# Kernel tuning notes

Hardware: AMD Instinct MI355X
Metric: run time of the kernel (lower is better)

Reference implementation:

```python
import jax, jax.numpy as jnp
import numpy as np

DIM = 512
HEADS = 8
HEAD_DIM = DIM // HEADS
SCALE = HEAD_DIM ** -0.5
CPB_HIDDEN = 512
N_CLASSES = 2
LN_EPS = 1e-5


def _layernorm(x, g, b):
    m = jnp.mean(x, axis=-1, keepdims=True)
    v = jnp.var(x, axis=-1, keepdims=True)
    return (x - m) / jnp.sqrt(v + LN_EPS) * g + b


def _coord_attention(x, coords, cpb_w1, cpb_b1, cpb_w2, cpb_b2, qkv_w, qkv_b, proj_w, proj_b):
    B, N, C = x.shape
    qkv = (x @ qkv_w + qkv_b).reshape(B, N, 3, HEADS, HEAD_DIM)
    q, k, v = jnp.moveaxis(qkv, 2, 0)  # each (B, N, H, hd)
    attn = jnp.einsum('bnhd,bmhd->bhnm', q * SCALE, k)  # (B, H, N, N)
    rel = coords[:, :, None, :] - coords[:, None, :, :]  # (B, N, N, 2)
    rel = rel / (jnp.linalg.norm(rel, axis=-1, keepdims=True) + 1e-6)
    bias = jax.nn.relu(rel @ cpb_w1 + cpb_b1) @ cpb_w2 + cpb_b2  # (B, N, N, H)
    attn = jax.nn.softmax(attn + jnp.transpose(bias, (0, 3, 1, 2)), axis=-1)
    out = jnp.einsum('bhnm,bmhd->bnhd', attn, v).reshape(B, N, C)
    return out @ proj_w + proj_b


def setup_inputs() -> dict:
    key = jax.random.key(0)
    ks = iter(jax.random.split(key, 32))
    d = {}
    d['h'] = jax.random.normal(next(ks), (1, 400, 1024), dtype=jnp.float32)
    d['coords'] = jax.random.uniform(next(ks), (1, 400, 2), dtype=jnp.float32) * 1000.0
    def lin(kw, kb, fan_in, fan_out):
        w = jax.random.normal(kw, (fan_in, fan_out), dtype=jnp.float32) / np.sqrt(fan_in)
        b = jax.random.normal(kb, (fan_out,), dtype=jnp.float32) * 0.01
        return w, b
    d['fc1_w'], d['fc1_b'] = lin(next(ks), next(ks), 1024, DIM)
    d['cls_token'] = jax.random.normal(next(ks), (1, 1, DIM), dtype=jnp.float32)
    for p in ('l1', 'l2'):
        d[p + '_norm_g'] = jnp.ones((DIM,), jnp.float32)
        d[p + '_norm_b'] = jnp.zeros((DIM,), jnp.float32)
        d[p + '_cpb_w1'], d[p + '_cpb_b1'] = lin(next(ks), next(ks), 2, CPB_HIDDEN)
        d[p + '_cpb_w2'], d[p + '_cpb_b2'] = lin(next(ks), next(ks), CPB_HIDDEN, HEADS)
        d[p + '_qkv_w'], d[p + '_qkv_b'] = lin(next(ks), next(ks), DIM, 3 * DIM)
        d[p + '_proj_w'], d[p + '_proj_b'] = lin(next(ks), next(ks), DIM, DIM)
    d['norm_g'] = jnp.ones((DIM,), jnp.float32)
    d['norm_b'] = jnp.zeros((DIM,), jnp.float32)
    d['fc2_w'], d['fc2_b'] = lin(next(ks), next(ks), DIM, N_CLASSES)
    return d


def reference(h, coords, fc1_w, fc1_b, cls_token,
              l1_norm_g, l1_norm_b, l1_cpb_w1, l1_cpb_b1, l1_cpb_w2, l1_cpb_b2,
              l1_qkv_w, l1_qkv_b, l1_proj_w, l1_proj_b,
              l2_norm_g, l2_norm_b, l2_cpb_w1, l2_cpb_b1, l2_cpb_w2, l2_cpb_b2,
              l2_qkv_w, l2_qkv_b, l2_proj_w, l2_proj_b,
              norm_g, norm_b, fc2_w, fc2_b):
    B, Np, _ = h.shape
    h = jax.nn.relu(h @ fc1_w + fc1_b)  # (B, N, 512)
    side = int(np.ceil(np.sqrt(Np)))
    add = side * side - Np  # pad bag to a perfect square (wrap-around copy)
    h = jnp.concatenate([h, h[:, :add, :]], axis=1)
    coords = jnp.concatenate([coords, coords[:, :add, :]], axis=1)
    cls = jnp.broadcast_to(cls_token, (B, 1, DIM))
    h = jnp.concatenate([cls, h], axis=1)
    coords = jnp.concatenate([jnp.zeros((B, 1, 2), h.dtype), coords], axis=1)
    h = h + _coord_attention(_layernorm(h, l1_norm_g, l1_norm_b), coords,
                             l1_cpb_w1, l1_cpb_b1, l1_cpb_w2, l1_cpb_b2,
                             l1_qkv_w, l1_qkv_b, l1_proj_w, l1_proj_b)
    h = h + _coord_attention(_layernorm(h, l2_norm_g, l2_norm_b), coords,
                             l2_cpb_w1, l2_cpb_b1, l2_cpb_w2, l2_cpb_b2,
                             l2_qkv_w, l2_qkv_b, l2_proj_w, l2_proj_b)
    h = _layernorm(h, norm_g, norm_b)[:, 0]  # CLS token
    return h @ fc2_w + fc2_b  # (B, n_classes)
```

## Files before the change

kernel.cpp:

```cpp
#include <hip/hip_runtime.h>
#include <math.h>

#define NP 401
#define DIM 512
#define LN_EPS 1e-5f
#define ATT_SCALE 0.125f
#define SP 448
#define PLANE (NP * SP)
#define CPB_M 16384
#define TSTRIDE (CPB_M + 64)
#define PQS (401L * 1536)
#define PVS (401L * 512)

template<bool TB, typename LA, typename LB>
__device__ __forceinline__ void gemm64(
    int kBeg, int kEnd, int tid,
    float (*as)[68], float (*bs)[68], float (&acc)[4][4],
    LA&& loadA, LB&& loadB)
{
    float aR[4], bR[4];
    loadA(kBeg, aR);
    loadB(kBeg, bR);
    for (int k0 = kBeg; k0 < kEnd; k0 += 16) {
        const int arow = tid >> 2, aq = tid & 3;
        as[aq * 4 + 0][arow] = aR[0];
        as[aq * 4 + 1][arow] = aR[1];
        as[aq * 4 + 2][arow] = aR[2];
        as[aq * 4 + 3][arow] = aR[3];
        if (!TB) {
            *(float4*)&bs[tid >> 4][(tid & 15) * 4] =
                make_float4(bR[0], bR[1], bR[2], bR[3]);
        } else {
            bs[aq * 4 + 0][arow] = bR[0];
            bs[aq * 4 + 1][arow] = bR[1];
            bs[aq * 4 + 2][arow] = bR[2];
            bs[aq * 4 + 3][arow] = bR[3];
        }
        __syncthreads();
        float nA[4] = {0.f,0.f,0.f,0.f}, nB[4] = {0.f,0.f,0.f,0.f};
        if (k0 + 16 < kEnd) { loadA(k0 + 16, nA); loadB(k0 + 16, nB); }
        const int tx = tid & 15, ty = tid >> 4;
        #pragma unroll
        for (int kk = 0; kk < 16; ++kk) {
            float4 a4 = *(const float4*)&as[kk][ty * 4];
            float4 b4 = *(const float4*)&bs[kk][tx * 4];
            float av[4] = {a4.x, a4.y, a4.z, a4.w};
            float bv[4] = {b4.x, b4.y, b4.z, b4.w};
            #pragma unroll
            for (int r = 0; r < 4; ++r)
                #pragma unroll
                for (int c = 0; c < 4; ++c)
                    acc[r][c] = fmaf(av[r], bv[c], acc[r][c]);
        }
        __syncthreads();
        #pragma unroll
        for (int j = 0; j < 4; ++j) { aR[j] = nA[j]; bR[j] = nB[j]; }
    }
}

__global__ __launch_bounds__(256) void gemm_split_kernel(
    const float* __restrict__ A, int lda,
    const float* __restrict__ B, int ldb,
    float* __restrict__ P, int ldc, long slice,
    int M, int N, int K, int skN)
{
    __shared__ float as[16][68], bs[16][68];
    const int tid = threadIdx.x;
    const int m0 = blockIdx.x * 64, n0 = blockIdx.y * 64;
    const int sk = blockIdx.z;
    const int KS = ((K + skN * 16 - 1) / (skN * 16)) * 16;
    const int kBeg = sk * KS;
    const int kEnd = (kBeg + KS < K) ? kBeg + KS : K;
    float acc[4][4] = {};

    auto loadA = [&](int k0, float r[4]) {
        r[0] = r[1] = r[2] = r[3] = 0.f;
        int gm = m0 + (tid >> 2);
        if (gm >= M) return;
        int gk = k0 + (tid & 3) * 4;
        const float* p = A + (long)gm * lda + gk;
        if (gk + 3 < kEnd) {
            float4 v = *(const float4*)p;
            r[0] = v.x; r[1] = v.y; r[2] = v.z; r[3] = v.w;
        } else {
            #pragma unroll
            for (int j = 0; j < 4; ++j) if (gk + j < kEnd) r[j] = p[j];
        }
    };
    auto loadB = [&](int k0, float r[4]) {
        r[0] = r[1] = r[2] = r[3] = 0.f;
        int gk = k0 + (tid >> 4);
        if (gk >= kEnd) return;
        int gn = n0 + (tid & 15) * 4;
        const float* p = B + (long)gk * ldb + gn;
        float4 v = *(const float4*)p;
        r[0] = v.x; r[1] = v.y; r[2] = v.z; r[3] = v.w;
    };
    if (kBeg < kEnd)
        gemm64<false>(kBeg, kEnd, tid, as, bs, acc, loadA, loadB);

    float* C = P + (long)sk * slice;
    const int tx = tid & 15, ty = tid >> 4;
    #pragma unroll
    for (int r = 0; r < 4; ++r) {
        int m = m0 + ty * 4 + r;
        if (m >= M) continue;
        *(float4*)&C[(long)m * ldc + n0 + tx * 4] =
            make_float4(acc[r][0], acc[r][1], acc[r][2], acc[r][3]);
    }
}

__global__ __launch_bounds__(256) void qk_kernel(
    const float* __restrict__ Pq, const float* __restrict__ qkvb,
    const int* __restrict__ pm, const float* __restrict__ pf,
    const float* __restrict__ T, float* __restrict__ S)
{
    __shared__ float as[16][68], bs[16][68];
    const int tid = threadIdx.x;
    const int m0 = blockIdx.x * 64, n0 = blockIdx.y * 64, h = blockIdx.z;
    float acc[4][4] = {};

    auto loadQ = [&](int k0, float r[4]) {
        int gm = m0 + (tid >> 2);
        if (gm > 400) { r[0]=r[1]=r[2]=r[3]=0.f; return; }
        int gk = k0 + (tid & 3) * 4;
        long off = (long)gm * 1536 + h * 64 + gk;
        float4 x0 = *(const float4*)(Pq + off);
        float4 x1 = *(const float4*)(Pq + PQS + off);
        float4 x2 = *(const float4*)(Pq + 2 * PQS + off);
        float4 x3 = *(const float4*)(Pq + 3 * PQS + off);
        float4 b  = *(const float4*)(qkvb + h * 64 + gk);
        r[0] = x0.x + x1.x + x2.x + x3.x + b.x;
        r[1] = x0.y + x1.y + x2.y + x3.y + b.y;
        r[2] = x0.z + x1.z + x2.z + x3.z + b.z;
        r[3] = x0.w + x1.w + x2.w + x3.w + b.w;
    };
    auto loadK = [&](int k0, float r[4]) {
        int gn = n0 + (tid >> 2);
        if (gn > 400) { r[0]=r[1]=r[2]=r[3]=0.f; return; }
        int gk = k0 + (tid & 3) * 4;
        long off = (long)gn * 1536 + 512 + h * 64 + gk;
        float4 x0 = *(const float4*)(Pq + off);
        float4 x1 = *(const float4*)(Pq + PQS + off);
        float4 x2 = *(const float4*)(Pq + 2 * PQS + off);
        float4 x3 = *(const float4*)(Pq + 3 * PQS + off);
        float4 b  = *(const float4*)(qkvb + 512 + h * 64 + gk);
        r[0] = x0.x + x1.x + x2.x + x3.x + b.x;
        r[1] = x0.y + x1.y + x2.y + x3.y + b.y;
        r[2] = x0.z + x1.z + x2.z + x3.z + b.z;
        r[3] = x0.w + x1.w + x2.w + x3.w + b.w;
    };
    gemm64<true>(0, 64, tid, as, bs, acc, loadQ, loadK);

    const int tx = tid & 15, ty = tid >> 4;
    const float* Tt = T + (long)h * TSTRIDE;
    float* Sp = S + (long)h * PLANE;
    #pragma unroll
    for (int r = 0; r < 4; ++r) {
        int i = m0 + ty * 4 + r;
        if (i > 400) continue;
        #pragma unroll
        for (int c = 0; c < 4; ++c) {
            int j = n0 + tx * 4 + c;
            if (j > 400) continue;
            int id = i * 416 + j;
            int mm = pm[id];
            float fr = pf[id];
            float t0 = Tt[mm], t1 = Tt[mm + 1];
            Sp[(long)i * SP + j] =
                fmaf(acc[r][c], ATT_SCALE, fmaf(fr, t1 - t0, t0));
        }
    }
}

__global__ __launch_bounds__(256) void softmax_kernel(float* __restrict__ S)
{
    int r = blockIdx.x * 4 + (threadIdx.x >> 6);
    if (r >= 3208) return;
    int hh = r / 401, i = r - hh * 401;
    float* row = S + (long)hh * PLANE + (long)i * SP;
    int lane = threadIdx.x & 63;
    float v[7], mx = -INFINITY;
    #pragma unroll
    for (int j = 0; j < 7; ++j) {
        int c = lane + j * 64;
        v[j] = (c < NP) ? row[c] : -INFINITY;
        mx = fmaxf(mx, v[j]);
    }
    #pragma unroll
    for (int off = 32; off > 0; off >>= 1)
        mx = fmaxf(mx, __shfl_xor(mx, off));
    float s = 0.f;
    #pragma unroll
    for (int j = 0; j < 7; ++j) {
        v[j] = (lane + j * 64 < NP) ? __expf(v[j] - mx) : 0.f;
        s += v[j];
    }
    #pragma unroll
    for (int off = 32; off > 0; off >>= 1)
        s += __shfl_xor(s, off);
    float inv = 1.f / s;
    #pragma unroll
    for (int j = 0; j < 7; ++j) {
        int c = lane + j * 64;
        if (c < NP) row[c] = v[j] * inv;
    }
}

__global__ __launch_bounds__(256) void pv_kernel(
    const float* __restrict__ S, const float* __restrict__ Pq,
    const float* __restrict__ qkvb, float* __restrict__ Pv)
{
    __shared__ float as[16][68], bs[16][68];
    const int tid = threadIdx.x;
    const int m0 = blockIdx.x * 64;
    const int h = blockIdx.z >> 2, sk = blockIdx.z & 3;
    const int kBeg = sk * 112;
    const int kEnd = (kBeg + 112 < NP) ? kBeg + 112 : NP;
    float acc[4][4] = {};

    auto loadA = [&](int k0, float r[4]) {
        r[0] = r[1] = r[2] = r[3] = 0.f;
        int gm = m0 + (tid >> 2);
        if (gm > 400) return;
        int gk = k0 + (tid & 3) * 4;
        const float* p = S + (long)h * PLANE + (long)gm * SP + gk;
        if (gk + 3 < kEnd) {
            float4 v = *(const float4*)p;
            r[0]=v.x; r[1]=v.y; r[2]=v.z; r[3]=v.w;
        } else {
            #pragma unroll
            for (int j = 0; j < 4; ++j) if (gk + j < kEnd) r[j] = p[j];
        }
    };
    auto loadB = [&](int k0, float r[4]) {
        r[0] = r[1] = r[2] = r[3] = 0.f;
        int key = k0 + (tid >> 4);
        if (key >= kEnd) return;
        int d = (tid & 15) * 4;
        long off = (long)key * 1536 + 1024 + h * 64 + d;
        float4 x0 = *(const float4*)(Pq + off);
        float4 x1 = *(const float4*)(Pq + PQS + off);
        float4 x2 = *(const float4*)(Pq + 2 * PQS + off);
        float4 x3 = *(const float4*)(Pq + 3 * PQS + off);
        float4 b  = *(const float4*)(qkvb + 1024 + h * 64 + d);
        r[0] = x0.x + x1.x + x2.x + x3.x + b.x;
        r[1] = x0.y + x1.y + x2.y + x3.y + b.y;
        r[2] = x0.z + x1.z + x2.z + x3.z + b.z;
        r[3] = x0.w + x1.w + x2.w + x3.w + b.w;
    };
    gemm64<false>(kBeg, kEnd, tid, as, bs, acc, loadA, loadB);

    float* C = Pv + (long)sk * PVS;
    const int tx = tid & 15, ty = tid >> 4;
    #pragma unroll
    for (int r = 0; r < 4; ++r) {
        int m = m0 + ty * 4 + r;
        if (m > 400) continue;
        *(float4*)&C[(long)m * 512 + h * 64 + tx * 4] =
            make_float4(acc[r][0], acc[r][1], acc[r][2], acc[r][3]);
    }
}

__global__ __launch_bounds__(256) void proj_kernel(
    const float* __restrict__ Pv, const float* __restrict__ projw,
    float* __restrict__ Pp)
{
    __shared__ float as[16][68], bs[16][68];
    const int tid = threadIdx.x;
    const int m0 = blockIdx.x * 64, n0 = blockIdx.y * 64, sk = blockIdx.z;
    const int kBeg = sk * 64, kEnd = kBeg + 64;
    float acc[4][4] = {};

    auto loadA = [&](int k0, float r[4]) {
        r[0] = r[1] = r[2] = r[3] = 0.f;
        int gm = m0 + (tid >> 2);
        if (gm > 400) return;
        int gk = k0 + (tid & 3) * 4;
        long off = (long)gm * 512 + gk;
        float4 x0 = *(const float4*)(Pv + off);
        float4 x1 = *(const float4*)(Pv + PVS + off);
        float4 x2 = *(const float4*)(Pv + 2 * PVS + off);
        float4 x3 = *(const float4*)(Pv + 3 * PVS + off);
        r[0] = x0.x + x1.x + x2.x + x3.x;
        r[1] = x0.y + x1.y + x2.y + x3.y;
        r[2] = x0.z + x1.z + x2.z + x3.z;
        r[3] = x0.w + x1.w + x2.w + x3.w;
    };
    auto loadB = [&](int k0, float r[4]) {
        int gk = k0 + (tid >> 4);
        int gn = n0 + (tid & 15) * 4;
        float4 v = *(const float4*)(projw + (long)gk * 512 + gn);
        r[0]=v.x; r[1]=v.y; r[2]=v.z; r[3]=v.w;
    };
    gemm64<false>(kBeg, kEnd, tid, as, bs, acc, loadA, loadB);

    float* C = Pp + (long)sk * PVS;
    const int tx = tid & 15, ty = tid >> 4;
    #pragma unroll
    for (int r = 0; r < 4; ++r) {
        int m = m0 + ty * 4 + r;
        if (m > 400) continue;
        *(float4*)&C[(long)m * 512 + n0 + tx * 4] =
            make_float4(acc[r][0], acc[r][1], acc[r][2], acc[r][3]);
    }
}

__global__ __launch_bounds__(256) void rowfuse_kernel(
    const float* __restrict__ P, long slice, int skN, int rowOff,
    const float* __restrict__ bias, int doRelu,
    const float* __restrict__ resid, const float* __restrict__ cls,
    float* __restrict__ h0,
    const float* __restrict__ g, const float* __restrict__ b,
    float* __restrict__ xln)
{
    const int r = blockIdx.x, t = threadIdx.x;
    float v0, v1;
    if (cls && r == 0) {
        v0 = cls[t]; v1 = cls[t + 256];
    } else {
        const float* p = P + (long)(r - rowOff) * DIM;
        v0 = bias[t]; v1 = bias[t + 256];
        for (int k = 0; k < skN; ++k) {
            v0 += p[(long)k * slice + t];
            v1 += p[(long)k * slice + t + 256];
        }
        if (resid) {
            v0 += resid[(long)r * DIM + t];
            v1 += resid[(long)r * DIM + t + 256];
        }
        if (doRelu) { v0 = fmaxf(v0, 0.f); v1 = fmaxf(v1, 0.f); }
    }
    h0[(long)r * DIM + t] = v0;
    h0[(long)r * DIM + t + 256] = v1;

    float s = v0 + v1, sq = v0 * v0 + v1 * v1;
    #pragma unroll
    for (int off = 32; off > 0; off >>= 1) {
        s += __shfl_down(s, off);
        sq += __shfl_down(sq, off);
    }
    __shared__ float ps[4], pq[4];
    int w = t >> 6, lane = t & 63;
    if (lane == 0) { ps[w] = s; pq[w] = sq; }
    __syncthreads();
    float Sm = ps[0] + ps[1] + ps[2] + ps[3];
    float Q = pq[0] + pq[1] + pq[2] + pq[3];
    float mean = Sm * (1.f / DIM);
    float var = Q * (1.f / DIM) - mean * mean;
    float inv = rsqrtf(var + LN_EPS);
    xln[(long)r * DIM + t]       = (v0 - mean) * inv * g[t] + b[t];
    xln[(long)r * DIM + t + 256] = (v1 - mean) * inv * g[t + 256] + b[t + 256];
}

__global__ __launch_bounds__(256) void cls_decode_kernel(
    const float* __restrict__ Pq, const float* __restrict__ qkvb,
    const int* __restrict__ pm, const float* __restrict__ pf,
    const float* __restrict__ T,
    float* __restrict__ cms, float* __restrict__ cpv)
{
    const int h = blockIdx.x, c = blockIdx.y, tid = threadIdx.x;
    const int kBeg = c * 64;
    __shared__ float q0[64], scraw[64], p[64], red[4][64], rr[2];

    if (tid < 64) {
        long o = h * 64 + tid;
        q0[tid] = Pq[o] + Pq[PQS + o] + Pq[2 * PQS + o] + Pq[3 * PQS + o]
                  + qkvb[o];
    }
    __syncthreads();

    {
        int k = tid >> 2, q = tid & 3;
        int j = kBeg + k;
        float dot = 0.f;
        if (j < NP) {
            long base = (long)j * 1536 + 512 + h * 64 + q * 16;
            #pragma unroll
            for (int d = 0; d < 16; d += 4) {
                float4 x0 = *(const float4*)(Pq + base + d);
                float4 x1 = *(const float4*)(Pq + PQS + base + d);
                float4 x2 = *(const float4*)(Pq + 2 * PQS + base + d);
                float4 x3 = *(const float4*)(Pq + 3 * PQS + base + d);
                float4 bb = *(const float4*)(qkvb + 512 + h * 64 + q * 16 + d);
                float4 qq = *(const float4*)(q0 + q * 16 + d);
                dot = fmaf(qq.x, x0.x + x1.x + x2.x + x3.x + bb.x, dot);
                dot = fmaf(qq.y, x0.y + x1.y + x2.y + x3.y + bb.y, dot);
                dot = fmaf(qq.z, x0.z + x1.z + x2.z + x3.z + bb.z, dot);
                dot = fmaf(qq.w, x0.w + x1.w + x2.w + x3.w + bb.w, dot);
            }
        }
        dot += __shfl_down(dot, 2);
        dot += __shfl_down(dot, 1);
        if (q == 0) scraw[k] = dot;
    }
    __syncthreads();

    if (tid < 64) {
        int j = kBeg + tid;
        float s;
        if (j < NP) {
            int mm = pm[j];
            float fr = pf[j];
            const float* Tt = T + (long)h * TSTRIDE;
            float t0 = Tt[mm], t1 = Tt[mm + 1];
            s = fmaf(scraw[tid], ATT_SCALE, fmaf(fr, t1 - t0, t0));
        } else {
            s = -INFINITY;
        }
        float m = s;
        #pragma unroll
        for (int off = 32; off > 0; off >>= 1)
            m = fmaxf(m, __shfl_xor(m, off));
        float e = (j < NP) ? __expf(s - m) : 0.f;
        float sum = e;
        #pragma unroll
        for (int off = 32; off > 0; off >>= 1)
            sum += __shfl_xor(sum, off);
        p[tid] = e;
        if (tid == 0) { rr[0] = m; rr[1] = sum; }
    }
    __syncthreads();

    {
        int w = tid >> 6, d = tid & 63;
        float vb = qkvb[1024 + h * 64 + d];
        float acc = 0.f;
        for (int k = w; k < 64; k += 4) {
            int j = kBeg + k;
            if (j >= NP) break;
            long o = (long)j * 1536 + 1024 + h * 64 + d;
            float v = Pq[o] + Pq[PQS + o] + Pq[2 * PQS + o] + Pq[3 * PQS + o]
                      + vb;
            acc = fmaf(p[k], v, acc);
        }
        red[w][d] = acc;
    }
    __syncthreads();
    if (tid < 64) {
        cpv[((long)h * 7 + c) * 64 + tid] =
            red[0][tid] + red[1][tid] + red[2][tid] + red[3][tid];
        if (tid == 0) {
            cms[(h * 7 + c) * 2 + 0] = rr[0];
            cms[(h * 7 + c) * 2 + 1] = rr[1];
        }
    }
}

__global__ __launch_bounds__(64) void cls_combine_kernel(
    const float* __restrict__ cms, const float* __restrict__ cpv,
    float* __restrict__ att0)
{
    int h = blockIdx.x, d = threadIdx.x;
    float M = -INFINITY;
    #pragma unroll
    for (int c = 0; c < 7; ++c)
        M = fmaxf(M, cms[(h * 7 + c) * 2]);
    float S = 0.f, acc = 0.f;
    #pragma unroll
    for (int c = 0; c < 7; ++c) {
        float e = __expf(cms[(h * 7 + c) * 2] - M);
        S += cms[(h * 7 + c) * 2 + 1] * e;
        acc += cpv[((long)h * 7 + c) * 64 + d] * e;
    }
    att0[h * 64 + d] = acc / S;
}

__global__ __launch_bounds__(256) void cls_proj_kernel(
    const float* __restrict__ att0, const float* __restrict__ projw,
    const float* __restrict__ projb, float* __restrict__ proj0)
{
    __shared__ float av[512], red[4][64];
    const int b = blockIdx.x, tid = threadIdx.x;
    av[tid] = att0[tid];
    av[tid + 256] = att0[tid + 256];
    __syncthreads();
    int g = tid >> 6, n = b * 64 + (tid & 63);
    float acc = 0.f;
    for (int k = g * 128; k < g * 128 + 128; ++k)
        acc = fmaf(av[k], projw[(long)k * 512 + n], acc);
    red[g][tid & 63] = acc;
    __syncthreads();
    if (tid < 64)
        proj0[b * 64 + tid] = red[0][tid] + red[1][tid] + red[2][tid]
                              + red[3][tid] + projb[b * 64 + tid];
}

__global__ __launch_bounds__(256) void cls_out_kernel(
    const float* __restrict__ h0, const float* __restrict__ proj0,
    const float* __restrict__ g, const float* __restrict__ b,
    const float* __restrict__ fc2w, const float* __restrict__ fc2b,
    float* __restrict__ out)
{
    const int t = threadIdx.x;
    float v0 = h0[t] + proj0[t];
    float v1 = h0[t + 256] + proj0[t + 256];
    float s = v0 + v1, sq = v0 * v0 + v1 * v1;
    #pragma unroll
    for (int off = 32; off > 0; off >>= 1) {
        s += __shfl_down(s, off);
        sq += __shfl_down(sq, off);
    }
    __shared__ float ps[4], pq[4], pc0[4], pc1[4];
    int w = t >> 6, lane = t & 63;
    if (lane == 0) { ps[w] = s; pq[w] = sq; }
    __syncthreads();
    float Sm = ps[0] + ps[1] + ps[2] + ps[3];
    float Q = pq[0] + pq[1] + pq[2] + pq[3];
    float mean = Sm * (1.f / DIM);
    float var = Q * (1.f / DIM) - mean * mean;
    float inv = rsqrtf(var + LN_EPS);
    float n0 = (v0 - mean) * inv * g[t] + b[t];
    float n1 = (v1 - mean) * inv * g[t + 256] + b[t + 256];
    float c0 = n0 * fc2w[t * 2]     + n1 * fc2w[(t + 256) * 2];
    float c1 = n0 * fc2w[t * 2 + 1] + n1 * fc2w[(t + 256) * 2 + 1];
    #pragma unroll
    for (int off = 32; off > 0; off >>= 1) {
        c0 += __shfl_down(c0, off);
        c1 += __shfl_down(c1, off);
    }
    if (lane == 0) { pc0[w] = c0; pc1[w] = c1; }
    __syncthreads();
    if (t == 0) {
        out[0] = pc0[0] + pc0[1] + pc0[2] + pc0[3] + fc2b[0];
        out[1] = pc1[0] + pc1[1] + pc1[2] + pc1[3] + fc2b[1];
    }
}

__global__ __launch_bounds__(256) void mega_kernel(
    const float* __restrict__ hin, const float* __restrict__ fc1_w,
    const float* __restrict__ w1_0, const float* __restrict__ b1_0,
    const float* __restrict__ w2_0, const float* __restrict__ b2_0,
    const float* __restrict__ w1_1, const float* __restrict__ b1_1,
    const float* __restrict__ w2_1, const float* __restrict__ b2_1,
    const float* __restrict__ coords,
    float* __restrict__ Pp, float* __restrict__ T,
    int* __restrict__ pm, float* __restrict__ pf)
{
    __shared__ float smem[2176];
    float (*as)[68] = (float(*)[68])smem;
    float (*bs)[68] = (float(*)[68])(smem + 1088);
    float (*red)[64][8] = (float(*)[64][8])smem;
    const int bid = blockIdx.x, tid = threadIdx.x;

    if (bid < 896) {
        int sk = bid / 56, rem = bid % 56;
        int m0 = (rem % 7) * 64, n0 = (rem / 7) * 64;
        int kBeg = sk * 64, kEnd = kBeg + 64;
        float acc[4][4] = {};
        auto loadA = [&](int k0, float r[4]) {
            r[0]=r[1]=r[2]=r[3]=0.f;
            int gm = m0 + (tid >> 2);
            if (gm >= 400) return;
            int gk = k0 + (tid & 3) * 4;
            float4 v = *(const float4*)(hin + (long)gm * 1024 + gk);
            r[0]=v.x; r[1]=v.y; r[2]=v.z; r[3]=v.w;
        };
        auto loadB = [&](int k0, float r[4]) {
            int gk = k0 + (tid >> 4);
            int gn = n0 + (tid & 15) * 4;
            float4 v = *(const float4*)(fc1_w + (long)gk * 512 + gn);
            r[0]=v.x; r[1]=v.y; r[2]=v.z; r[3]=v.w;
        };
        gemm64<false>(kBeg, kEnd, tid, as, bs, acc, loadA, loadB);
        float* C = Pp + (long)sk * PVS;
        const int tx = tid & 15, ty = tid >> 4;
        #pragma unroll
        for (int r = 0; r < 4; ++r) {
            int m = m0 + ty * 4 + r;
            if (m >= 400) continue;
            *(float4*)&C[(long)m * 512 + n0 + tx * 4] =
                make_float4(acc[r][0], acc[r][1], acc[r][2], acc[r][3]);
        }
    } else if (bid < 1410) {
        int tb = bid - 896;
        int z = tb / 257, ab = tb % 257;
        const float* w1 = z ? w1_1 : w1_0;
        const float* b1 = z ? b1_1 : b1_0;
        const float* w2 = z ? w2_1 : w2_0;
        const float* b2 = z ? b2_1 : b2_0;
        const int lane = tid & 63, wv = tid >> 6;
        float ca = 0.f, sa = 0.f;
        if (ab != 256) {
            float th = fmaf((float)(ab * 64 + lane),
                            (float)(2.0 * M_PI / CPB_M), -(float)M_PI);
            sincosf(th, &sa, &ca);
        } else if (lane == 0) {
            sincosf((float)M_PI, &sa, &ca);
        }
        float a8[8] = {};
        const int kbeg = wv * 128;
        #pragma unroll 4
        for (int k = kbeg; k < kbeg + 128; ++k) {
            float hk = fmaxf(fmaf(ca, w1[k],
                                  fmaf(sa, w1[512 + k], b1[k])), 0.f);
            #pragma unroll
            for (int h2 = 0; h2 < 8; ++h2)
                a8[h2] = fmaf(hk, w2[k * 8 + h2], a8[h2]);
        }
        #pragma unroll
        for (int h2 = 0; h2 < 8; ++h2) red[wv][lane][h2] = a8[h2];
        __syncthreads();
        if (tid < 64) {
            int aidx = ab * 64 + tid;
            #pragma unroll
            for (int h2 = 0; h2 < 8; ++h2)
                T[(long)(z * 8 + h2) * TSTRIDE + aidx] =
                    red[0][tid][h2] + red[1][tid][h2] +
                    red[2][tid][h2] + red[3][tid][h2] + b2[h2];
        }
    } else {
        int p = (bid - 1410) * 256 + tid;
        if (p < NP * NP) {
            int i = p / NP, j = p - i * NP;
            float xi = (i == 0) ? 0.f : coords[(i - 1) * 2];
            float yi = (i == 0) ? 0.f : coords[(i - 1) * 2 + 1];
            float xj = (j == 0) ? 0.f : coords[(j - 1) * 2];
            float yj = (j == 0) ? 0.f : coords[(j - 1) * 2 + 1];
            float rx = xi - xj, ry = yi - yj;
            int mm; float fr;
            if (rx == 0.f && ry == 0.f) {
                mm = CPB_M + 1; fr = 0.f;
            } else {
                float x = (atan2f(ry, rx) + 3.14159265358979f)
                          * (float)(CPB_M / (2.0 * M_PI));
                int mi = (int)x;
                fr = x - (float)mi;
                mm = (mi >= CPB_M) ? mi - CPB_M : mi;
            }
            pm[i * 416 + j] = mm;
            pf[i * 416 + j] = fr;
        }
    }
}

extern "C" void kernel_launch(void* const* d_in, const int* in_sizes, int n_in,
                              void* d_out, int out_size, void* d_ws, size_t ws_size,
                              hipStream_t stream)
{
    const float* coords = (const float*)d_in[1];
    float* ws = (float*)d_ws;
    float* h0   = ws;                    ws += 401L * 512;
    float* xln  = ws;                    ws += 401L * 512;
    float* S    = ws;                    ws += 8L * PLANE;
    float* T    = ws;                    ws += 16L * TSTRIDE;
    int*   pm   = (int*)ws;              ws += 401L * 416;
    float* pf   = ws;                    ws += 401L * 416;
    float* Pq   = ws;                    ws += 4L * PQS;
    float* Pv   = ws;                    ws += 4L * PVS;
    float* Pp   = ws;                    ws += 16L * PVS;
    float* att0 = ws;                    ws += 512;
    float* proj0 = ws;                   ws += 512;
    float* cms  = ws;                    ws += 8L * 7 * 2;
    float* cpv  = ws;                    ws += 8L * 7 * 64;

    mega_kernel<<<2039, 256, 0, stream>>>(
        (const float*)d_in[0], (const float*)d_in[2],
        (const float*)d_in[7],  (const float*)d_in[8],
        (const float*)d_in[9],  (const float*)d_in[10],
        (const float*)d_in[17], (const float*)d_in[18],
        (const float*)d_in[19], (const float*)d_in[20],
        coords, Pp, T, pm, pf);

    rowfuse_kernel<<<401, 256, 0, stream>>>(
        Pp, PVS, 16, 1, (const float*)d_in[3], 1, nullptr,
        (const float*)d_in[4], h0,
        (const float*)d_in[5], (const float*)d_in[6], xln);

    gemm_split_kernel<<<dim3(7, 24, 4), 256, 0, stream>>>(
        xln, 512, (const float*)d_in[11], 1536, Pq, 1536, PQS,
        401, 1536, 512, 4);
    qk_kernel<<<dim3(7, 7, 8), 256, 0, stream>>>(
        Pq, (const float*)d_in[12], pm, pf, T, S);
    softmax_kernel<<<802, 256, 0, stream>>>(S);
    pv_kernel<<<dim3(7, 1, 32), 256, 0, stream>>>(
        S, Pq, (const float*)d_in[12], Pv);
    proj_kernel<<<dim3(7, 8, 8), 256, 0, stream>>>(
        Pv, (const float*)d_in[13], Pp);
    rowfuse_kernel<<<401, 256, 0, stream>>>(
        Pp, PVS, 8, 0, (const float*)d_in[14], 0, h0, nullptr, h0,
        (const float*)d_in[15], (const float*)d_in[16], xln);

    gemm_split_kernel<<<dim3(7, 24, 4), 256, 0, stream>>>(
        xln, 512, (const float*)d_in[21], 1536, Pq, 1536, PQS,
        401, 1536, 512, 4);
    cls_decode_kernel<<<dim3(8, 7), 256, 0, stream>>>(
        Pq, (const float*)d_in[22], pm, pf, T + 8L * TSTRIDE, cms, cpv);
    cls_combine_kernel<<<8, 64, 0, stream>>>(cms, cpv, att0);
    cls_proj_kernel<<<8, 256, 0, stream>>>(
        att0, (const float*)d_in[23], (const float*)d_in[24], proj0);
    cls_out_kernel<<<1, 256, 0, stream>>>(
        h0, proj0, (const float*)d_in[25], (const float*)d_in[26],
        (const float*)d_in[27], (const float*)d_in[28], (float*)d_out);
}
```

Baseline: 263.9 us.

## Reduce split-K partials once in a dedicated kernel; fold cls combine into proj

```diff
diff --git a/kernel.cpp b/kernel.cpp
--- a/kernel.cpp
+++ b/kernel.cpp
@@ -110,8 +110,27 @@
     }
 }
 
+__global__ __launch_bounds__(256) void reduce_kernel(
+    const float* __restrict__ P, long slice, int skN,
+    const float* __restrict__ bias, float* __restrict__ out,
+    int total, int N)
+{
+    int idx = (blockIdx.x * 256 + threadIdx.x) * 4;
+    if (idx >= total) return;
+    float4 s = *(const float4*)(P + idx);
+    for (int k = 1; k < skN; ++k) {
+        float4 p = *(const float4*)(P + (long)k * slice + idx);
+        s.x += p.x; s.y += p.y; s.z += p.z; s.w += p.w;
+    }
+    if (bias) {
+        const float4 b = *(const float4*)(bias + (idx % N));
+        s.x += b.x; s.y += b.y; s.z += b.z; s.w += b.w;
+    }
+    *(float4*)(out + idx) = s;
+}
+
 __global__ __launch_bounds__(256) void qk_kernel(
-    const float* __restrict__ Pq, const float* __restrict__ qkvb,
+    const float* __restrict__ qkv,
     const int* __restrict__ pm, const float* __restrict__ pf,
     const float* __restrict__ T, float* __restrict__ S)
 {
@@ -124,31 +143,15 @@
         int gm = m0 + (tid >> 2);
         if (gm > 400) { r[0]=r[1]=r[2]=r[3]=0.f; return; }
         int gk = k0 + (tid & 3) * 4;
-        long off = (long)gm * 1536 + h * 64 + gk;
-        float4 x0 = *(const float4*)(Pq + off);
-        float4 x1 = *(const float4*)(Pq + PQS + off);
-        float4 x2 = *(const float4*)(Pq + 2 * PQS + off);
-        float4 x3 = *(const float4*)(Pq + 3 * PQS + off);
-        float4 b  = *(const float4*)(qkvb + h * 64 + gk);
-        r[0] = x0.x + x1.x + x2.x + x3.x + b.x;
-        r[1] = x0.y + x1.y + x2.y + x3.y + b.y;
-        r[2] = x0.z + x1.z + x2.z + x3.z + b.z;
-        r[3] = x0.w + x1.w + x2.w + x3.w + b.w;
+        float4 v = *(const float4*)(qkv + (long)gm * 1536 + h * 64 + gk);
+        r[0]=v.x; r[1]=v.y; r[2]=v.z; r[3]=v.w;
     };
     auto loadK = [&](int k0, float r[4]) {
         int gn = n0 + (tid >> 2);
         if (gn > 400) { r[0]=r[1]=r[2]=r[3]=0.f; return; }
         int gk = k0 + (tid & 3) * 4;
-        long off = (long)gn * 1536 + 512 + h * 64 + gk;
-        float4 x0 = *(const float4*)(Pq + off);
-        float4 x1 = *(const float4*)(Pq + PQS + off);
-        float4 x2 = *(const float4*)(Pq + 2 * PQS + off);
-        float4 x3 = *(const float4*)(Pq + 3 * PQS + off);
-        float4 b  = *(const float4*)(qkvb + 512 + h * 64 + gk);
-        r[0] = x0.x + x1.x + x2.x + x3.x + b.x;
-        r[1] = x0.y + x1.y + x2.y + x3.y + b.y;
-        r[2] = x0.z + x1.z + x2.z + x3.z + b.z;
-        r[3] = x0.w + x1.w + x2.w + x3.w + b.w;
+        float4 v = *(const float4*)(qkv + (long)gn * 1536 + 512 + h * 64 + gk);
+        r[0]=v.x; r[1]=v.y; r[2]=v.z; r[3]=v.w;
     };
     gemm64<true>(0, 64, tid, as, bs, acc, loadQ, loadK);
 
@@ -208,8 +211,8 @@
 }
 
 __global__ __launch_bounds__(256) void pv_kernel(
-    const float* __restrict__ S, const float* __restrict__ Pq,
-    const float* __restrict__ qkvb, float* __restrict__ Pv)
+    const float* __restrict__ S, const float* __restrict__ qkv,
+    float* __restrict__ Pv)
 {
     __shared__ float as[16][68], bs[16][68];
     const int tid = threadIdx.x;
@@ -238,16 +241,8 @@
         int key = k0 + (tid >> 4);
         if (key >= kEnd) return;
         int d = (tid & 15) * 4;
-        long off = (long)key * 1536 + 1024 + h * 64 + d;
-        float4 x0 = *(const float4*)(Pq + off);
-        float4 x1 = *(const float4*)(Pq + PQS + off);
-        float4 x2 = *(const float4*)(Pq + 2 * PQS + off);
-        float4 x3 = *(const float4*)(Pq + 3 * PQS + off);
-        float4 b  = *(const float4*)(qkvb + 1024 + h * 64 + d);
-        r[0] = x0.x + x1.x + x2.x + x3.x + b.x;
-        r[1] = x0.y + x1.y + x2.y + x3.y + b.y;
-        r[2] = x0.z + x1.z + x2.z + x3.z + b.z;
-        r[3] = x0.w + x1.w + x2.w + x3.w + b.w;
+        float4 v = *(const float4*)(qkv + (long)key * 1536 + 1024 + h * 64 + d);
+        r[0]=v.x; r[1]=v.y; r[2]=v.z; r[3]=v.w;
     };
     gemm64<false>(kBeg, kEnd, tid, as, bs, acc, loadA, loadB);
 
@@ -263,7 +258,7 @@
 }
 
 __global__ __launch_bounds__(256) void proj_kernel(
-    const float* __restrict__ Pv, const float* __restrict__ projw,
+    const float* __restrict__ att, const float* __restrict__ projw,
     float* __restrict__ Pp)
 {
     __shared__ float as[16][68], bs[16][68];
@@ -277,15 +272,8 @@
         int gm = m0 + (tid >> 2);
         if (gm > 400) return;
         int gk = k0 + (tid & 3) * 4;
-        long off = (long)gm * 512 + gk;
-        float4 x0 = *(const float4*)(Pv + off);
-        float4 x1 = *(const float4*)(Pv + PVS + off);
-        float4 x2 = *(const float4*)(Pv + 2 * PVS + off);
-        float4 x3 = *(const float4*)(Pv + 3 * PVS + off);
-        r[0] = x0.x + x1.x + x2.x + x3.x;
-        r[1] = x0.y + x1.y + x2.y + x3.y;
-        r[2] = x0.z + x1.z + x2.z + x3.z;
-        r[3] = x0.w + x1.w + x2.w + x3.w;
+        float4 v = *(const float4*)(att + (long)gm * 512 + gk);
+        r[0]=v.x; r[1]=v.y; r[2]=v.z; r[3]=v.w;
     };
     auto loadB = [&](int k0, float r[4]) {
         int gk = k0 + (tid >> 4);
@@ -354,7 +342,7 @@
 }
 
 __global__ __launch_bounds__(256) void cls_decode_kernel(
-    const float* __restrict__ Pq, const float* __restrict__ qkvb,
+    const float* __restrict__ qkv,
     const int* __restrict__ pm, const float* __restrict__ pf,
     const float* __restrict__ T,
     float* __restrict__ cms, float* __restrict__ cpv)
@@ -363,11 +351,7 @@
     const int kBeg = c * 64;
     __shared__ float q0[64], scraw[64], p[64], red[4][64], rr[2];
 
-    if (tid < 64) {
-        long o = h * 64 + tid;
-        q0[tid] = Pq[o] + Pq[PQS + o] + Pq[2 * PQS + o] + Pq[3 * PQS + o]
-                  + qkvb[o];
-    }
+    if (tid < 64) q0[tid] = qkv[h * 64 + tid];
     __syncthreads();
 
     {
@@ -375,19 +359,16 @@
         int j = kBeg + k;
         float dot = 0.f;
         if (j < NP) {
-            long base = (long)j * 1536 + 512 + h * 64 + q * 16;
+            const float* kp = qkv + (long)j * 1536 + 512 + h * 64 + q * 16;
+            const float* qp = q0 + q * 16;
             #pragma unroll
             for (int d = 0; d < 16; d += 4) {
-                float4 x0 = *(const float4*)(Pq + base + d);
-                float4 x1 = *(const float4*)(Pq + PQS + base + d);
-                float4 x2 = *(const float4*)(Pq + 2 * PQS + base + d);
-                float4 x3 = *(const float4*)(Pq + 3 * PQS + base + d);
-                float4 bb = *(const float4*)(qkvb + 512 + h * 64 + q * 16 + d);
-                float4 qq = *(const float4*)(q0 + q * 16 + d);
-                dot = fmaf(qq.x, x0.x + x1.x + x2.x + x3.x + bb.x, dot);
-                dot = fmaf(qq.y, x0.y + x1.y + x2.y + x3.y + bb.y, dot);
-                dot = fmaf(qq.z, x0.z + x1.z + x2.z + x3.z + bb.z, dot);
-                dot = fmaf(qq.w, x0.w + x1.w + x2.w + x3.w + bb.w, dot);
+                float4 kv = *(const float4*)(kp + d);
+                float4 qq = *(const float4*)(qp + d);
+                dot = fmaf(qq.x, kv.x, dot);
+                dot = fmaf(qq.y, kv.y, dot);
+                dot = fmaf(qq.z, kv.z, dot);
+                dot = fmaf(qq.w, kv.w, dot);
             }
         }
         dot += __shfl_down(dot, 2);
@@ -424,15 +405,11 @@
 
     {
         int w = tid >> 6, d = tid & 63;
-        float vb = qkvb[1024 + h * 64 + d];
         float acc = 0.f;
         for (int k = w; k < 64; k += 4) {
             int j = kBeg + k;
             if (j >= NP) break;
-            long o = (long)j * 1536 + 1024 + h * 64 + d;
-            float v = Pq[o] + Pq[PQS + o] + Pq[2 * PQS + o] + Pq[3 * PQS + o]
-                      + vb;
-            acc = fmaf(p[k], v, acc);
+            acc = fmaf(p[k], qkv[(long)j * 1536 + 1024 + h * 64 + d], acc);
         }
         red[w][d] = acc;
     }
@@ -447,33 +424,28 @@
     }
 }
 
-__global__ __launch_bounds__(64) void cls_combine_kernel(
+__global__ __launch_bounds__(256) void cls_proj_kernel(
     const float* __restrict__ cms, const float* __restrict__ cpv,
-    float* __restrict__ att0)
-{
-    int h = blockIdx.x, d = threadIdx.x;
-    float M = -INFINITY;
-    #pragma unroll
-    for (int c = 0; c < 7; ++c)
-        M = fmaxf(M, cms[(h * 7 + c) * 2]);
-    float S = 0.f, acc = 0.f;
-    #pragma unroll
-    for (int c = 0; c < 7; ++c) {
-        float e = __expf(cms[(h * 7 + c) * 2] - M);
-        S += cms[(h * 7 + c) * 2 + 1] * e;
-        acc += cpv[((long)h * 7 + c) * 64 + d] * e;
-    }
-    att0[h * 64 + d] = acc / S;
-}
-
-__global__ __launch_bounds__(256) void cls_proj_kernel(
-    const float* __restrict__ att0, const float* __restrict__ projw,
-    const float* __restrict__ projb, float* __restrict__ proj0)
+    const float* __restrict__ projw, const float* __restrict__ projb,
+    float* __restrict__ proj0)
 {
     __shared__ float av[512], red[4][64];
     const int b = blockIdx.x, tid = threadIdx.x;
-    av[tid] = att0[tid];
-    av[tid + 256] = att0[tid + 256];
+    for (int d = tid; d < 512; d += 256) {
+        int h = d >> 6, dd = d & 63;
+        float M = -INFINITY;
+        #pragma unroll
+        for (int c = 0; c < 7; ++c)
+            M = fmaxf(M, cms[(h * 7 + c) * 2]);
+        float S = 0.f, acc = 0.f;
+        #pragma unroll
+        for (int c = 0; c < 7; ++c) {
+            float e = __expf(cms[(h * 7 + c) * 2] - M);
+            S += cms[(h * 7 + c) * 2 + 1] * e;
+            acc += cpv[((long)h * 7 + c) * 64 + dd] * e;
+        }
+        av[d] = acc / S;
+    }
     __syncthreads();
     int g = tid >> 6, n = b * 64 + (tid & 63);
     float acc = 0.f;
@@ -647,9 +619,10 @@
     int*   pm   = (int*)ws;              ws += 401L * 416;
     float* pf   = ws;                    ws += 401L * 416;
     float* Pq   = ws;                    ws += 4L * PQS;
+    float* qkv  = ws;                    ws += 401L * 1536;
     float* Pv   = ws;                    ws += 4L * PVS;
+    float* att  = ws;                    ws += 401L * 512;
     float* Pp   = ws;                    ws += 16L * PVS;
-    float* att0 = ws;                    ws += 512;
     float* proj0 = ws;                   ws += 512;
     float* cms  = ws;                    ws += 8L * 7 * 2;
     float* cpv  = ws;                    ws += 8L * 7 * 64;
@@ -670,13 +643,15 @@
     gemm_split_kernel<<<dim3(7, 24, 4), 256, 0, stream>>>(
         xln, 512, (const float*)d_in[11], 1536, Pq, 1536, PQS,
         401, 1536, 512, 4);
-    qk_kernel<<<dim3(7, 7, 8), 256, 0, stream>>>(
-        Pq, (const float*)d_in[12], pm, pf, T, S);
+    reduce_kernel<<<602, 256, 0, stream>>>(
+        Pq, PQS, 4, (const float*)d_in[12], qkv, 401 * 1536, 1536);
+    qk_kernel<<<dim3(7, 7, 8), 256, 0, stream>>>(qkv, pm, pf, T, S);
     softmax_kernel<<<802, 256, 0, stream>>>(S);
-    pv_kernel<<<dim3(7, 1, 32), 256, 0, stream>>>(
-        S, Pq, (const float*)d_in[12], Pv);
+    pv_kernel<<<dim3(7, 1, 32), 256, 0, stream>>>(S, qkv, Pv);
+    reduce_kernel<<<201, 256, 0, stream>>>(
+        Pv, PVS, 4, nullptr, att, 401 * 512, 512);
     proj_kernel<<<dim3(7, 8, 8), 256, 0, stream>>>(
-        Pv, (const float*)d_in[13], Pp);
+        att, (const float*)d_in[13], Pp);
     rowfuse_kernel<<<401, 256, 0, stream>>>(
         Pp, PVS, 8, 0, (const float*)d_in[14], 0, h0, nullptr, h0,
         (const float*)d_in[15], (const float*)d_in[16], xln);
@@ -684,11 +659,12 @@
     gemm_split_kernel<<<dim3(7, 24, 4), 256, 0, stream>>>(
         xln, 512, (const float*)d_in[21], 1536, Pq, 1536, PQS,
         401, 1536, 512, 4);
+    reduce_kernel<<<602, 256, 0, stream>>>(
+        Pq, PQS, 4, (const float*)d_in[22], qkv, 401 * 1536, 1536);
     cls_decode_kernel<<<dim3(8, 7), 256, 0, stream>>>(
-        Pq, (const float*)d_in[22], pm, pf, T + 8L * TSTRIDE, cms, cpv);
-    cls_combine_kernel<<<8, 64, 0, stream>>>(cms, cpv, att0);
+        qkv, pm, pf, T + 8L * TSTRIDE, cms, cpv);
     cls_proj_kernel<<<8, 256, 0, stream>>>(
-        att0, (const float*)d_in[23], (const float*)d_in[24], proj0);
+        cms, cpv, (const float*)d_in[23], (const float*)d_in[24], proj0);
     cls_out_kernel<<<1, 256, 0, stream>>>(
         h0, proj0, (const float*)d_in[25], (const float*)d_in[26],
         (const float*)d_in[27], (const float*)d_in[28], (float*)d_out);
```

After: 250.4 us. -5.1%, faster.
